# Performance work log

Hardware: AMD Instinct MI355X
Metric: run time of the kernel (lower is better)

Reference implementation:

```python
import jax, jax.numpy as jnp
import numpy as np

B, N, F_IN, F_OUT = 8, 2048, 64, 64
ALPHA = 0.2  # LeakyReLU negative slope
LN_EPS = 1e-5
NEG_BIG = -9e15


def setup_inputs() -> dict:
    key = jax.random.key(0)
    ks = jax.random.split(key, 8)
    inp = {}
    inp["input"] = jax.random.normal(ks[0], (B, N, F_IN), dtype=jnp.float32)
    inp["adj"] = jax.random.randint(ks[1], (N, N), 0, 2, dtype=jnp.int32)
    # parameters (kaiming/xavier approximated with scaled normals)
    inp["W"] = jax.random.normal(ks[2], (F_IN, F_OUT), dtype=jnp.float32) * np.sqrt(2.0 / F_OUT)
    inp["a"] = jax.random.normal(ks[3], (2 * F_OUT, 1), dtype=jnp.float32) * np.sqrt(2.0 / (2 * F_OUT + 1))
    inp["node_weights"] = jax.random.normal(ks[4], (N,), dtype=jnp.float32)
    inp["node_bias"] = jnp.zeros((N,), dtype=jnp.float32)
    inp["ln_gamma"] = jnp.ones((F_OUT,), dtype=jnp.float32)
    inp["ln_beta"] = jnp.zeros((F_OUT,), dtype=jnp.float32)
    return inp


def reference(input, adj, W, a, node_weights, node_bias, ln_gamma, ln_beta):
    # eval mode: dropout is identity
    # node-wise affine + residual
    x = input * node_weights[None, :, None] + node_bias[None, :, None] + input
    # linear projection + LayerNorm over features
    h = jnp.matmul(x, W)  # [B, N, F_OUT]
    mu = jnp.mean(h, axis=-1, keepdims=True)
    var = jnp.mean(jnp.square(h - mu), axis=-1, keepdims=True)
    h = (h - mu) * jax.lax.rsqrt(var + LN_EPS) * ln_gamma + ln_beta
    # additive GAT scores WITHOUT materializing [B,N,N,2F]:
    # e_ij = LeakyReLU(h_i . a1 + h_j . a2), identical math to cat([h_i,h_j]) @ a
    a1 = a[:F_OUT, 0]
    a2 = a[F_OUT:, 0]
    s1 = jnp.einsum("bnf,f->bn", h, a1)  # [B, N]
    s2 = jnp.einsum("bnf,f->bn", h, a2)  # [B, N]
    e = jax.nn.leaky_relu(s1[:, :, None] + s2[:, None, :], negative_slope=ALPHA)
    # masked softmax over neighbors (last axis)
    mask = (adj > 0)[None, :, :]  # [1, N, N] broadcast over batch
    att = jax.nn.softmax(jnp.where(mask, e, NEG_BIG), axis=-1)
    # weighted aggregation + residual, then ELU (concat=True)
    h_prime = jnp.matmul(att, h) + h
    return jax.nn.elu(h_prime)
```

## Files before the change

### kernel.cpp

```cpp
#include <hip/hip_runtime.h>
#include <math.h>

#define Bb 8
#define Nn 2048
#define ALPHA 0.2f
#define LN_EPS 1e-5f
#define LOG2E 1.4426950408889634f

typedef __attribute__((ext_vector_type(8))) short short8;
typedef __attribute__((ext_vector_type(4))) float f32x4;
typedef __attribute__((ext_vector_type(4))) int int4v;

__device__ inline unsigned short f2bf(float f) {
    unsigned u = __builtin_bit_cast(unsigned, f);
    u += 0x7fffu + ((u >> 16) & 1u);
    return (unsigned short)(u >> 16);
}

__device__ __forceinline__ void gll16(const void* g, void* l) {
    __builtin_amdgcn_global_load_lds(
        (const __attribute__((address_space(1))) unsigned int*)g,
        (__attribute__((address_space(3))) unsigned int*)l, 16, 0, 0);
}

__global__ __launch_bounds__(256) void prep(
    const int* __restrict__ adj,
    const float* __restrict__ in, const float* __restrict__ W,
    const float* __restrict__ a, const float* __restrict__ nw,
    const float* __restrict__ nb, const float* __restrict__ gam,
    const float* __restrict__ bet,
    unsigned int* __restrict__ bitsT,
    float* __restrict__ h, float* __restrict__ s1L, float* __restrict__ s2L,
    unsigned short* __restrict__ hT2)
{
    __shared__ unsigned char rowb[256];
    int bid = blockIdx.x, t = threadIdx.x;

    if (bid < Nn) {
        int i = bid;
        const int4* arow = (const int4*)(adj + (size_t)i * Nn);
        int4 v0 = arow[t * 2], v1 = arow[t * 2 + 1];
        unsigned by = (unsigned)(v0.x > 0)       | ((unsigned)(v0.y > 0) << 1)
                    | ((unsigned)(v0.z > 0) << 2) | ((unsigned)(v0.w > 0) << 3)
                    | ((unsigned)(v1.x > 0) << 4) | ((unsigned)(v1.y > 0) << 5)
                    | ((unsigned)(v1.z > 0) << 6) | ((unsigned)(v1.w > 0) << 7);
        rowb[t] = (unsigned char)by;
        __syncthreads();
        if (t < 64) {
            unsigned w32;
            __builtin_memcpy(&w32, &rowb[t * 4], 4);
            bitsT[((size_t)(i >> 4) * 64 + t) * 16 + (i & 15)] = w32;
        }
        return;
    }

    int lane = t & 63, wv = t >> 6;
    int am = lane & 15, ag = lane >> 4;
    int node0 = (bid - Nn) * 64 + wv * 16;
    int b = node0 >> 11;
    int n0 = node0 & (Nn - 1);

    short8 wf[4][2];
#pragma unroll
    for (int cb = 0; cb < 4; ++cb)
#pragma unroll
        for (int kh = 0; kh < 2; ++kh)
#pragma unroll
            for (int e = 0; e < 8; ++e)
                wf[cb][kh][e] = (short)f2bf(W[(kh * 32 + 8 * ag + e) * 64 + cb * 16 + am]);

    int nrow = n0 + am;
    float nwv = nw[nrow] + 1.0f, nbv = nb[nrow];
    const float* xrow = in + (size_t)(node0 + am) * 64 + 8 * ag;
    short8 xa0, xa1;
#pragma unroll
    for (int e = 0; e < 8; ++e) {
        xa0[e] = (short)f2bf(xrow[e] * nwv + nbv);
        xa1[e] = (short)f2bf(xrow[32 + e] * nwv + nbv);
    }

    f32x4 acc0 = {0,0,0,0}, acc1 = {0,0,0,0}, acc2 = {0,0,0,0}, acc3 = {0,0,0,0};
    acc0 = __builtin_amdgcn_mfma_f32_16x16x32_bf16(xa0, wf[0][0], acc0, 0, 0, 0);
    acc1 = __builtin_amdgcn_mfma_f32_16x16x32_bf16(xa0, wf[1][0], acc1, 0, 0, 0);
    acc2 = __builtin_amdgcn_mfma_f32_16x16x32_bf16(xa0, wf[2][0], acc2, 0, 0, 0);
    acc3 = __builtin_amdgcn_mfma_f32_16x16x32_bf16(xa0, wf[3][0], acc3, 0, 0, 0);
    acc0 = __builtin_amdgcn_mfma_f32_16x16x32_bf16(xa1, wf[0][1], acc0, 0, 0, 0);
    acc1 = __builtin_amdgcn_mfma_f32_16x16x32_bf16(xa1, wf[1][1], acc1, 0, 0, 0);
    acc2 = __builtin_amdgcn_mfma_f32_16x16x32_bf16(xa1, wf[2][1], acc2, 0, 0, 0);
    acc3 = __builtin_amdgcn_mfma_f32_16x16x32_bf16(xa1, wf[3][1], acc3, 0, 0, 0);

    float mu[4], rsq[4];
#pragma unroll
    for (int q = 0; q < 4; ++q) {
        float s = (acc0[q] + acc1[q]) + (acc2[q] + acc3[q]);
        s += __shfl_xor(s, 1, 64); s += __shfl_xor(s, 2, 64);
        s += __shfl_xor(s, 4, 64); s += __shfl_xor(s, 8, 64);
        mu[q] = s * (1.f / 64.f);
    }
#pragma unroll
    for (int q = 0; q < 4; ++q) {
        float d0 = acc0[q] - mu[q], d1 = acc1[q] - mu[q];
        float d2 = acc2[q] - mu[q], d3 = acc3[q] - mu[q];
        float ss = (d0 * d0 + d1 * d1) + (d2 * d2 + d3 * d3);
        ss += __shfl_xor(ss, 1, 64); ss += __shfl_xor(ss, 2, 64);
        ss += __shfl_xor(ss, 4, 64); ss += __shfl_xor(ss, 8, 64);
        rsq[q] = rsqrtf(ss * (1.f / 64.f) + LN_EPS);
    }
    float gl0 = gam[am], gl1 = gam[16 + am], gl2 = gam[32 + am], gl3 = gam[48 + am];
    float bl0 = bet[am], bl1 = bet[16 + am], bl2 = bet[32 + am], bl3 = bet[48 + am];
    f32x4 hn0, hn1, hn2, hn3;
#pragma unroll
    for (int q = 0; q < 4; ++q) {
        hn0[q] = (acc0[q] - mu[q]) * rsq[q] * gl0 + bl0;
        hn1[q] = (acc1[q] - mu[q]) * rsq[q] * gl1 + bl1;
        hn2[q] = (acc2[q] - mu[q]) * rsq[q] * gl2 + bl2;
        hn3[q] = (acc3[q] - mu[q]) * rsq[q] * gl3 + bl3;
    }

    float a10 = a[am], a11 = a[16 + am], a12 = a[32 + am], a13 = a[48 + am];
    float a20 = a[64 + am], a21 = a[80 + am], a22 = a[96 + am], a23 = a[112 + am];
    float s1p[4], s2p[4];
#pragma unroll
    for (int q = 0; q < 4; ++q) {
        float s1v = (hn0[q] * a10 + hn1[q] * a11) + (hn2[q] * a12 + hn3[q] * a13);
        float s2v = (hn0[q] * a20 + hn1[q] * a21) + (hn2[q] * a22 + hn3[q] * a23);
        s1v += __shfl_xor(s1v, 1, 64); s1v += __shfl_xor(s1v, 2, 64);
        s1v += __shfl_xor(s1v, 4, 64); s1v += __shfl_xor(s1v, 8, 64);
        s2v += __shfl_xor(s2v, 1, 64); s2v += __shfl_xor(s2v, 2, 64);
        s2v += __shfl_xor(s2v, 4, 64); s2v += __shfl_xor(s2v, 8, 64);
        s1p[q] = s1v; s2p[q] = s2v;
    }
    if (am == 0) {
#pragma unroll
        for (int q = 0; q < 4; ++q) {
            s1L[node0 + ag * 4 + q] = s1p[q] * LOG2E;
            s2L[node0 + ag * 4 + q] = s2p[q] * LOG2E;
        }
    }

#pragma unroll
    for (int q = 0; q < 4; ++q) {
        float* hp = h + (size_t)(node0 + ag * 4 + q) * 64 + am;
        hp[0] = hn0[q]; hp[16] = hn1[q]; hp[32] = hn2[q]; hp[48] = hn3[q];
    }

    int jw = n0 >> 5;
    int AG2 = ((n0 & 31) >> 3) + (ag >> 1);
    int e0 = (ag & 1) * 4;
    size_t fbase = ((size_t)((b * 64 + jw) * 4)) * 512 + (AG2 * 16 + am) * 8 + e0;
#pragma unroll
    for (int cb = 0; cb < 4; ++cb) {
        f32x4 hc = cb == 0 ? hn0 : cb == 1 ? hn1 : cb == 2 ? hn2 : hn3;
        unsigned short v[4] = {f2bf(hc[0]), f2bf(hc[1]), f2bf(hc[2]), f2bf(hc[3])};
        *(uint2*)&hT2[fbase + (size_t)cb * 512] = *(uint2*)v;
    }
}

__global__ __launch_bounds__(256) void attention9(
    const float* __restrict__ h, const unsigned short* __restrict__ hT2,
    const float* __restrict__ s1L, const float* __restrict__ s2L,
    const unsigned int* __restrict__ bitsT, float* __restrict__ out)
{
    __shared__ __align__(16) unsigned short frag[2][4][4][512];
    __shared__ __align__(16) unsigned int mask_lds[2][64][16];
    __shared__ __align__(16) float s2l[2048];

    int t = threadIdx.x, wv = t >> 6, lane = t & 63;
    int am = lane & 15, ag = lane >> 4;
    int rr = wv & 1, js = wv >> 1;
    int bx = blockIdx.x, b = blockIdx.y;

    float s1r = s1L[b * Nn + bx * 32 + rr * 16 + am];
    const unsigned int* msrc = bitsT + (size_t)(bx * 2) * 1024;
    const float* ssrc = s2L + b * Nn;
    const unsigned short* slab = hT2 + (size_t)b * 131072;

#pragma unroll
    for (int k = 0; k < 2; ++k) {
        int sl = wv * 2 + k;
        gll16(msrc + sl * 256 + lane * 4, &((unsigned int*)mask_lds)[sl * 256]);
        gll16(ssrc + sl * 256 + lane * 4, &s2l[sl * 256]);
    }
#pragma unroll
    for (int fb = 0; fb < 4; ++fb)
        gll16(slab + (size_t)(wv * 4 + fb) * 512 + lane * 8, &frag[0][wv][fb][0]);
    asm volatile("s_waitcnt vmcnt(0)" ::: "memory");
    __builtin_amdgcn_s_barrier();

    f32x4 acc0 = {0,0,0,0}, acc1 = {0,0,0,0}, acc2 = {0,0,0,0}, acc3 = {0,0,0,0};
    f32x4 accz = {0,0,0,0};
    const short8 vone = {(short)0x3F80, (short)0x3F80, (short)0x3F80, (short)0x3F80,
                         (short)0x3F80, (short)0x3F80, (short)0x3F80, (short)0x3F80};

#pragma unroll
    for (int st = 0; st < 16; ++st) {
        if (st < 15) {
            int gw = (st + 1) * 4 + wv;
#pragma unroll
            for (int fb = 0; fb < 4; ++fb)
                gll16(slab + (size_t)(gw * 4 + fb) * 512 + lane * 8,
                      &frag[(st + 1) & 1][wv][fb][0]);
        }
#pragma unroll
        for (int wi = 0; wi < 2; ++wi) {
            int wls = js * 2 + wi;
            int wl = st * 4 + wls;
            unsigned wd = mask_lds[rr][wl][am];
            float4 sa = *(const float4*)&s2l[wl * 32 + 8 * ag];
            float4 sb = *(const float4*)&s2l[wl * 32 + 8 * ag + 4];
            float se[8] = {sa.x, sa.y, sa.z, sa.w, sb.x, sb.y, sb.z, sb.w};
            float p[8];
#pragma unroll
            for (int e = 0; e < 8; ++e) {
                float x = s1r + se[e];
                float lr = fmaxf(x, ALPHA * x);
                float ev = __builtin_amdgcn_exp2f(lr);
                p[e] = ((wd >> (8 * ag + e)) & 1u) ? ev : 0.f;
            }
            int4v aw;
            aw.x = __builtin_amdgcn_perm(__builtin_bit_cast(unsigned, p[1]),
                                         __builtin_bit_cast(unsigned, p[0]), 0x07060302u);
            aw.y = __builtin_amdgcn_perm(__builtin_bit_cast(unsigned, p[3]),
                                         __builtin_bit_cast(unsigned, p[2]), 0x07060302u);
            aw.z = __builtin_amdgcn_perm(__builtin_bit_cast(unsigned, p[5]),
                                         __builtin_bit_cast(unsigned, p[4]), 0x07060302u);
            aw.w = __builtin_amdgcn_perm(__builtin_bit_cast(unsigned, p[7]),
                                         __builtin_bit_cast(unsigned, p[6]), 0x07060302u);
            short8 af = __builtin_bit_cast(short8, aw);
            short8 f0 = *(const short8*)&frag[st & 1][wls][0][lane * 8];
            short8 f1 = *(const short8*)&frag[st & 1][wls][1][lane * 8];
            short8 f2 = *(const short8*)&frag[st & 1][wls][2][lane * 8];
            short8 f3 = *(const short8*)&frag[st & 1][wls][3][lane * 8];
            acc0 = __builtin_amdgcn_mfma_f32_16x16x32_bf16(af, f0, acc0, 0, 0, 0);
            acc1 = __builtin_amdgcn_mfma_f32_16x16x32_bf16(af, f1, acc1, 0, 0, 0);
            acc2 = __builtin_amdgcn_mfma_f32_16x16x32_bf16(af, f2, acc2, 0, 0, 0);
            acc3 = __builtin_amdgcn_mfma_f32_16x16x32_bf16(af, f3, acc3, 0, 0, 0);
            accz = __builtin_amdgcn_mfma_f32_16x16x32_bf16(af, vone, accz, 0, 0, 0);
        }
        asm volatile("s_waitcnt vmcnt(0)" ::: "memory");
        __builtin_amdgcn_s_barrier();
    }

    float* ep  = (float*)&frag[0][0][0][0];
    float* zep = (float*)&frag[1][0][0][0];
#pragma unroll
    for (int q = 0; q < 4; ++q) {
        int rloc = rr * 16 + 4 * ag + q;
        ep[(js * 32 + rloc) * 64 +  0 + am] = acc0[q];
        ep[(js * 32 + rloc) * 64 + 16 + am] = acc1[q];
        ep[(js * 32 + rloc) * 64 + 32 + am] = acc2[q];
        ep[(js * 32 + rloc) * 64 + 48 + am] = acc3[q];
        if (am == 0) zep[js * 32 + rloc] = accz[q];
    }
    __syncthreads();

    int rl = t >> 3, fo = (t & 7) * 8;
    float zinv = 1.f / (zep[rl] + zep[32 + rl]);
    size_t base = ((size_t)(b * Nn + bx * 32 + rl)) * 64 + fo;
    const float* e0p = &ep[rl * 64 + fo];
    const float* e1p = &ep[(32 + rl) * 64 + fo];
    float4 h0 = *(const float4*)&h[base];
    float4 h1 = *(const float4*)&h[base + 4];
    float4 o0, o1;
    o0.x = (e0p[0] + e1p[0]) * zinv + h0.x; o0.x = o0.x > 0.f ? o0.x : expm1f(o0.x);
    o0.y = (e0p[1] + e1p[1]) * zinv + h0.y; o0.y = o0.y > 0.f ? o0.y : expm1f(o0.y);
    o0.z = (e0p[2] + e1p[2]) * zinv + h0.z; o0.z = o0.z > 0.f ? o0.z : expm1f(o0.z);
    o0.w = (e0p[3] + e1p[3]) * zinv + h0.w; o0.w = o0.w > 0.f ? o0.w : expm1f(o0.w);
    o1.x = (e0p[4] + e1p[4]) * zinv + h1.x; o1.x = o1.x > 0.f ? o1.x : expm1f(o1.x);
    o1.y = (e0p[5] + e1p[5]) * zinv + h1.y; o1.y = o1.y > 0.f ? o1.y : expm1f(o1.y);
    o1.z = (e0p[6] + e1p[6]) * zinv + h1.z; o1.z = o1.z > 0.f ? o1.z : expm1f(o1.z);
    o1.w = (e0p[7] + e1p[7]) * zinv + h1.w; o1.w = o1.w > 0.f ? o1.w : expm1f(o1.w);
    *(float4*)&out[base] = o0;
    *(float4*)&out[base + 4] = o1;
}

extern "C" void kernel_launch(void* const* d_in, const int* in_sizes, int n_in,
                              void* d_out, int out_size, void* d_ws, size_t ws_size,
                              hipStream_t stream) {
    const float* in  = (const float*)d_in[0];
    const int*   adj = (const int*)d_in[1];
    const float* W   = (const float*)d_in[2];
    const float* a   = (const float*)d_in[3];
    const float* nw  = (const float*)d_in[4];
    const float* nb  = (const float*)d_in[5];
    const float* gam = (const float*)d_in[6];
    const float* bet = (const float*)d_in[7];
    float* out = (float*)d_out;

    char* ws = (char*)d_ws;
    float* h   = (float*)ws;
    float* s1L = (float*)(ws + (size_t)Bb * Nn * 64 * 4);
    float* s2L = s1L + (size_t)Bb * Nn;
    unsigned int* bitsT = (unsigned int*)(s2L + (size_t)Bb * Nn);
    unsigned short* hT2 = (unsigned short*)(bitsT + (size_t)Nn * Nn / 32);

    hipLaunchKernelGGL(prep, dim3(Nn + Bb * Nn / 64), dim3(256), 0, stream,
                       adj, in, W, a, nw, nb, gam, bet, bitsT, h, s1L, s2L, hT2);
    hipLaunchKernelGGL(attention9, dim3(Nn / 32, Bb), dim3(256), 0, stream,
                       h, hT2, s1L, s2L, bitsT, out);
}
```

Before: 33.49 us.

## Factor exp of LeakyReLU score into per-row and per-column exponentials

The attention kernel now precomputes exp2(s2) and exp2(0.2*s2) per column into shared memory and exp2(s1), exp2(0.2*s1) per row. Each score becomes max(E1p*E2p, E1n*E2n), which replaces a per-element exp with two multiplies and a max. This relies on exp being monotonic and on LeakyReLU being the max of two linear terms, and it can overflow if scores are large since there is no max subtraction. Block indexing in both kernels is also remapped so that consecutive blocks cycle over batches, which may change cache locality. The extra 16KB of LDS may lower occupancy.

```diff
diff --git a/kernel.cpp b/kernel.cpp
--- a/kernel.cpp
+++ b/kernel.cpp
@@ -56,8 +56,9 @@
 
     int lane = t & 63, wv = t >> 6;
     int am = lane & 15, ag = lane >> 4;
-    int node0 = (bid - Nn) * 64 + wv * 16;
-    int b = node0 >> 11;
+    int k = bid - Nn;
+    int b = k & 7, c = k >> 3;
+    int node0 = b * Nn + c * 64 + wv * 16;
     int n0 = node0 & (Nn - 1);
 
     short8 wf[4][2];
@@ -164,13 +165,17 @@
     __shared__ __align__(16) unsigned short frag[2][4][4][512];
     __shared__ __align__(16) unsigned int mask_lds[2][64][16];
     __shared__ __align__(16) float s2l[2048];
+    __shared__ __align__(16) float s2e[2048 * 2];
 
     int t = threadIdx.x, wv = t >> 6, lane = t & 63;
     int am = lane & 15, ag = lane >> 4;
     int rr = wv & 1, js = wv >> 1;
-    int bx = blockIdx.x, b = blockIdx.y;
+    int id = blockIdx.x;
+    int b = id & 7, bx = id >> 3;
 
     float s1r = s1L[b * Nn + bx * 32 + rr * 16 + am];
+    float E1p = __builtin_amdgcn_exp2f(s1r);
+    float E1n = __builtin_amdgcn_exp2f(0.2f * s1r);
     const unsigned int* msrc = bitsT + (size_t)(bx * 2) * 1024;
     const float* ssrc = s2L + b * Nn;
     const unsigned short* slab = hT2 + (size_t)b * 131072;
@@ -187,6 +192,15 @@
     asm volatile("s_waitcnt vmcnt(0)" ::: "memory");
     __builtin_amdgcn_s_barrier();
 
+#pragma unroll
+    for (int k = 0; k < 8; ++k) {
+        int j = t * 8 + k;
+        float v = s2l[j];
+        s2e[j * 2]     = __builtin_amdgcn_exp2f(v);
+        s2e[j * 2 + 1] = __builtin_amdgcn_exp2f(0.2f * v);
+    }
+    __syncthreads();
+
     f32x4 acc0 = {0,0,0,0}, acc1 = {0,0,0,0}, acc2 = {0,0,0,0}, acc3 = {0,0,0,0};
     f32x4 accz = {0,0,0,0};
     const short8 vone = {(short)0x3F80, (short)0x3F80, (short)0x3F80, (short)0x3F80,
@@ -206,17 +220,23 @@
             int wls = js * 2 + wi;
             int wl = st * 4 + wls;
             unsigned wd = mask_lds[rr][wl][am];
-            float4 sa = *(const float4*)&s2l[wl * 32 + 8 * ag];
-            float4 sb = *(const float4*)&s2l[wl * 32 + 8 * ag + 4];
-            float se[8] = {sa.x, sa.y, sa.z, sa.w, sb.x, sb.y, sb.z, sb.w};
+            const float* qb = &s2e[(wl * 32 + 8 * ag) * 2];
+            float4 q0 = *(const float4*)&qb[0];
+            float4 q1 = *(const float4*)&qb[4];
+            float4 q2 = *(const float4*)&qb[8];
+            float4 q3 = *(const float4*)&qb[12];
             float p[8];
-#pragma unroll
-            for (int e = 0; e < 8; ++e) {
-                float x = s1r + se[e];
-                float lr = fmaxf(x, ALPHA * x);
-                float ev = __builtin_amdgcn_exp2f(lr);
-                p[e] = ((wd >> (8 * ag + e)) & 1u) ? ev : 0.f;
-            }
+            p[0] = fmaxf(E1p * q0.x, E1n * q0.y);
+            p[1] = fmaxf(E1p * q0.z, E1n * q0.w);
+            p[2] = fmaxf(E1p * q1.x, E1n * q1.y);
+            p[3] = fmaxf(E1p * q1.z, E1n * q1.w);
+            p[4] = fmaxf(E1p * q2.x, E1n * q2.y);
+            p[5] = fmaxf(E1p * q2.z, E1n * q2.w);
+            p[6] = fmaxf(E1p * q3.x, E1n * q3.y);
+            p[7] = fmaxf(E1p * q3.z, E1n * q3.w);
+#pragma unroll
+            for (int e = 0; e < 8; ++e)
+                p[e] = ((wd >> (8 * ag + e)) & 1u) ? p[e] : 0.f;
             int4v aw;
             aw.x = __builtin_amdgcn_perm(__builtin_bit_cast(unsigned, p[1]),
                                          __builtin_bit_cast(unsigned, p[0]), 0x07060302u);
@@ -296,6 +316,6 @@
 
     hipLaunchKernelGGL(prep, dim3(Nn + Bb * Nn / 64), dim3(256), 0, stream,
                        adj, in, W, a, nw, nb, gam, bet, bitsT, h, s1L, s2L, hT2);
-    hipLaunchKernelGGL(attention9, dim3(Nn / 32, Bb), dim3(256), 0, stream,
+    hipLaunchKernelGGL(attention9, dim3(512), dim3(256), 0, stream,
                        h, hT2, s1L, s2L, bitsT, out);
 }
```

Result: faster. 29.01 us, median of 2 (-13.4%).
